# Kernel tuning notes

Measured on AMD Instinct MI355X. Metric: run time of the kernel, lower is better.

The kernel has to match this reference:

```python
import jax, jax.numpy as jnp
import numpy as np

THRESHOLD = 0.5
NEG_POS = 3
ALPHA = 1.0


def cxcy_to_xy(c):
    return jnp.concatenate([c[..., :2] - c[..., 2:] / 2, c[..., :2] + c[..., 2:] / 2], -1)


def xy_to_cxcy(b):
    return jnp.concatenate([(b[..., :2] + b[..., 2:]) / 2, b[..., 2:] - b[..., :2]], -1)


def compute_iou(a, b):
    # a: (M,4) xyxy, b: (D,4) xyxy -> (M,D)
    lt = jnp.maximum(a[:, None, :2], b[None, :, :2])
    rb = jnp.minimum(a[:, None, 2:], b[None, :, 2:])
    wh = jnp.clip(rb - lt, 0.0)
    inter = wh[..., 0] * wh[..., 1]
    area_a = (a[:, 2] - a[:, 0]) * (a[:, 3] - a[:, 1])
    area_b = (b[:, 2] - b[:, 0]) * (b[:, 3] - b[:, 1])
    return inter / (area_a[:, None] + area_b[None, :] - inter)


def encode_bboxes(g_cxcy, priors_cxcy):
    # standard SSD encoding with variances (0.1, 0.2)
    return jnp.concatenate([
        (g_cxcy[:, :2] - priors_cxcy[:, :2]) / (priors_cxcy[:, 2:] / 10.0),
        jnp.log(g_cxcy[:, 2:] / priors_cxcy[:, 2:]) * 5.0,
    ], -1)


def match_one(boxes, labels, priors_xy, priors_cxcy):
    # boxes: (M,4) xyxy, labels: (M,)
    M = boxes.shape[0]
    overlaps = compute_iou(boxes, priors_xy)                 # (M, D)
    overlaps_per_default = overlaps.max(axis=0)              # (D,)
    objects_per_default = overlaps.argmax(axis=0)            # (D,)
    defaults_per_gt = overlaps.argmax(axis=1)                # (M,)
    # force-match each gt to its best prior
    objects_per_default = objects_per_default.at[defaults_per_gt].set(jnp.arange(M))
    overlaps_per_default = overlaps_per_default.at[defaults_per_gt].set(1.0)
    lab = labels[objects_per_default]                        # (D,)
    lab = jnp.where(overlaps_per_default < THRESHOLD, 0, lab)
    matched = boxes[objects_per_default]                     # (D,4)
    loc_t = encode_bboxes(xy_to_cxcy(matched), priors_cxcy)  # (D,4)
    return loc_t, lab


def setup_inputs() -> dict:
    key = jax.random.key(0)
    ks = jax.random.split(key, 7)
    B, D, M, C = 128, 8732, 32, 21
    p_c = jax.random.uniform(ks[0], (D, 2), minval=0.05, maxval=0.95)
    p_wh = jax.random.uniform(ks[1], (D, 2), minval=0.02, maxval=0.4)
    default_boxes = jnp.concatenate([p_c, p_wh], -1)         # cxcy priors
    g_c = jax.random.uniform(ks[2], (B, M, 2), minval=0.2, maxval=0.8)
    g_wh = jax.random.uniform(ks[3], (B, M, 2), minval=0.05, maxval=0.3)
    gt_boxes = jnp.clip(jnp.concatenate([g_c - g_wh / 2, g_c + g_wh / 2], -1), 0.0, 1.0)
    gt_labels = jax.random.randint(ks[4], (B, M), 1, C)
    loc_pred = jax.random.normal(ks[5], (B, D, 4), dtype=jnp.float32)
    cls_pred = jax.random.normal(ks[6], (B, D, C), dtype=jnp.float32)
    return {"loc_pred": loc_pred, "cls_pred": cls_pred, "gt_boxes": gt_boxes,
            "gt_labels": gt_labels, "default_boxes": default_boxes}


def reference(loc_pred, cls_pred, gt_boxes, gt_labels, default_boxes):
    priors_xy = cxcy_to_xy(default_boxes)
    loc_t, conf_t = jax.vmap(match_one, in_axes=(0, 0, None, None))(
        gt_boxes, gt_labels, priors_xy, default_boxes)      # (B,D,4), (B,D)
    pos = conf_t > 0                                         # (B,D)
    n_pos = pos.sum(axis=1)                                  # (B,)
    n_total = jnp.maximum(n_pos.sum(), 1).astype(loc_pred.dtype)

    # localization: smooth-L1 summed over positives
    d = loc_pred - loc_t
    ad = jnp.abs(d)
    sl1 = jnp.where(ad < 1.0, 0.5 * d * d, ad - 0.5).sum(-1)  # (B,D)
    loc_loss = jnp.where(pos, sl1, 0.0).sum()

    # confidence: CE with hard negative mining (neg:pos = 3)
    logp = jax.nn.log_softmax(cls_pred, axis=-1)
    ce = -jnp.take_along_axis(logp, conf_t[..., None], axis=-1)[..., 0]  # (B,D)
    ce_neg = jnp.where(pos, 0.0, ce)
    order = jnp.argsort(-ce_neg, axis=1)
    rank = jnp.argsort(order, axis=1)                        # hardness rank per row
    n_neg = NEG_POS * n_pos                                  # (B,)
    neg_mask = (rank < n_neg[:, None]) & (~pos)
    conf_loss = jnp.where(pos | neg_mask, ce, 0.0).sum()

    return (conf_loss + ALPHA * loc_loss) / n_total
```

## Files before the change

### kernel.cpp

```cpp
#include <hip/hip_runtime.h>

#define BB 128
#define DD 8732
#define MM 32
#define CC 21

constexpr int K1_PR  = 4;
constexpr int K1_CH  = 256 * K1_PR;
constexpr int K1_NCH = (DD + K1_CH - 1) / K1_CH;
constexpr int K2_CELLS = 256;
constexpr int K2_NBLK  = (DD + K2_CELLS - 1) / K2_CELLS;
constexpr int K2B_T    = 1024;
constexpr int K2B_PER  = (DD + K2B_T - 1) / K2B_T;
constexpr int K2B_W    = K2B_T / 64;

constexpr size_t WS_DPG    = 0;
constexpr size_t WS_ROW    = 32768;
constexpr int    ROW_STRIDE = 16;
constexpr size_t WS_GSUM   = 40960;
constexpr size_t WS_GNPOS  = 41088;
constexpr size_t WS_DONE   = 41216;
constexpr size_t WS_ZERO_BYTES = 41344;
constexpr size_t WS_PACKED = 41472;
constexpr size_t WS_CENEG  = WS_PACKED + (size_t)BB * DD * 4;

__device__ __forceinline__ float wave_sum_f(float v) {
#pragma unroll
  for (int o = 32; o > 0; o >>= 1) v += __shfl_xor(v, o, 64);
  return v;
}
__device__ __forceinline__ int wave_sum_i(int v) {
#pragma unroll
  for (int o = 32; o > 0; o >>= 1) v += __shfl_xor(v, o, 64);
  return v;
}

__global__ __launch_bounds__(256) void k1_match(
    const float* __restrict__ gt_boxes, const int* __restrict__ gt_labels,
    const float* __restrict__ dboxes,
    unsigned int* __restrict__ packed, unsigned long long* __restrict__ dpg) {
  __shared__ float s_gx1[MM], s_gy1[MM], s_gx2[MM], s_gy2[MM], s_ga[MM];
  __shared__ int s_gl[MM];
  __shared__ unsigned long long s_pm[MM * 4];

  const int b = blockIdx.y;
  const int tid = threadIdx.x;
  if (tid < MM) {
    const float* g = gt_boxes + ((size_t)b * MM + tid) * 4;
    const float x1 = g[0], y1 = g[1], x2 = g[2], y2 = g[3];
    s_gx1[tid] = x1; s_gy1[tid] = y1; s_gx2[tid] = x2; s_gy2[tid] = y2;
    s_ga[tid] = __fmul_rn(__fsub_rn(x2, x1), __fsub_rn(y2, y1));
    s_gl[tid] = gt_labels[b * MM + tid];
  }
  __syncthreads();

  float px1[K1_PR], py1[K1_PR], px2[K1_PR], py2[K1_PR], pa[K1_PR];
  int dd[K1_PR];
  const int dbase = blockIdx.x * K1_CH + tid;
#pragma unroll
  for (int i = 0; i < K1_PR; ++i) {
    const int d = dbase + i * 256;
    if (d < DD) {
      const float4 p = *(const float4*)(dboxes + (size_t)d * 4);
      const float hw = __fmul_rn(p.z, 0.5f), hh = __fmul_rn(p.w, 0.5f);
      px1[i] = __fsub_rn(p.x, hw); py1[i] = __fsub_rn(p.y, hh);
      px2[i] = __fadd_rn(p.x, hw); py2[i] = __fadd_rn(p.y, hh);
      pa[i] = __fmul_rn(__fsub_rn(px2[i], px1[i]), __fsub_rn(py2[i], py1[i]));
      dd[i] = d;
    } else {
      px1[i] = 3e9f; py1[i] = 3e9f; px2[i] = 3e9f; py2[i] = 3e9f; pa[i] = 1.0f;
      dd[i] = 0x7FFFFFFF;
    }
  }

  float vb[K1_PR]; int mb[K1_PR];
#pragma unroll
  for (int i = 0; i < K1_PR; ++i) { vb[i] = -1.0f; mb[i] = 0; }

  const int lane = tid & 63, wid = tid >> 6;
  for (int m = 0; m < MM; ++m) {
    const float gx1 = s_gx1[m], gy1 = s_gy1[m], gx2 = s_gx2[m], gy2 = s_gy2[m];
    const float ga = s_ga[m];
    float mv = -1.0f; int md = 0x7FFFFFFF;
#pragma unroll
    for (int i = 0; i < K1_PR; ++i) {
      const float w = fmaxf(0.0f, __fsub_rn(fminf(gx2, px2[i]), fmaxf(gx1, px1[i])));
      const float h = fmaxf(0.0f, __fsub_rn(fminf(gy2, py2[i]), fmaxf(gy1, py1[i])));
      const float inter = __fmul_rn(w, h);
      const float den = __fsub_rn(__fadd_rn(ga, pa[i]), inter);
      const float val = __fdiv_rn(inter, den);
      if (val > vb[i]) { vb[i] = val; mb[i] = m; }
      if (val > mv) { mv = val; md = dd[i]; }
    }
    unsigned long long key =
        (((unsigned long long)__float_as_uint(mv)) << 32) |
        (unsigned long long)(0xFFFFFFFFu - (unsigned)md);
#pragma unroll
    for (int o = 32; o > 0; o >>= 1) {
      const unsigned long long other = __shfl_xor(key, o, 64);
      if (other > key) key = other;
    }
    if (lane == 0) s_pm[m * 4 + wid] = key;
  }
  __syncthreads();
  if (tid < MM) {
    unsigned long long k0 = s_pm[tid * 4 + 0];
    if (s_pm[tid * 4 + 1] > k0) k0 = s_pm[tid * 4 + 1];
    if (s_pm[tid * 4 + 2] > k0) k0 = s_pm[tid * 4 + 2];
    if (s_pm[tid * 4 + 3] > k0) k0 = s_pm[tid * 4 + 3];
    atomicMax(&dpg[b * MM + tid], k0);
  }
#pragma unroll
  for (int i = 0; i < K1_PR; ++i) {
    if (dd[i] < DD) {
      const int lab = (vb[i] < 0.5f) ? 0 : s_gl[mb[i]];
      packed[(size_t)b * DD + dd[i]] = ((unsigned)lab << 8) | (unsigned)mb[i];
    }
  }
}

__global__ __launch_bounds__(256) void k2a_ce(
    const float* __restrict__ loc_pred, const float* __restrict__ cls_pred,
    const float* __restrict__ gt_boxes, const int* __restrict__ gt_labels,
    const float* __restrict__ dboxes, const unsigned int* __restrict__ packed,
    const unsigned long long* __restrict__ dpg, float* __restrict__ ce_neg,
    float* __restrict__ rowacc) {
  __shared__ float s_cls[K2_CELLS * CC];
  __shared__ int s_dstar[MM], s_lab[MM];
  __shared__ float s_gt[MM][4];
  __shared__ float s_rf[4], s_rl[4];
  __shared__ int s_ri[4];

  const int b = blockIdx.y;
  const int d0 = blockIdx.x * K2_CELLS;
  const int tid = threadIdx.x;
  const int ncell = min(K2_CELLS, DD - d0);
  const int nflt = ncell * CC;
  const float* srcf = cls_pred + ((size_t)b * DD + d0) * CC;
  const int nv4 = nflt >> 2;
  for (int i = tid; i < nv4; i += 256)
    ((float4*)s_cls)[i] = ((const float4*)srcf)[i];
  for (int i = (nv4 << 2) + tid; i < nflt; i += 256) s_cls[i] = srcf[i];

  if (tid < MM) {
    s_dstar[tid] = (int)(0xFFFFFFFFu - (unsigned)(dpg[b * MM + tid] & 0xFFFFFFFFull));
    s_lab[tid] = gt_labels[b * MM + tid];
    const float4 g = *(const float4*)(gt_boxes + ((size_t)b * MM + tid) * 4);
    s_gt[tid][0] = g.x; s_gt[tid][1] = g.y; s_gt[tid][2] = g.z; s_gt[tid][3] = g.w;
  }
  __syncthreads();

  float ce_pos = 0.0f, sl1 = 0.0f; int posc = 0;
  if (tid < ncell) {
    const int d = d0 + tid;
    const unsigned p = packed[(size_t)b * DD + d];
    int bm = (int)(p & 255u), lab = (int)(p >> 8);
#pragma unroll
    for (int m = 0; m < MM; ++m)
      if (s_dstar[m] == d) { bm = m; lab = s_lab[m]; }
    const float* x = &s_cls[tid * CC];
    float mx = x[0];
#pragma unroll
    for (int c = 1; c < CC; ++c) mx = fmaxf(mx, x[c]);
    float se = 0.0f;
#pragma unroll
    for (int c = 0; c < CC; ++c) se = __fadd_rn(se, __expf(__fsub_rn(x[c], mx)));
    const float ce = __fsub_rn(__fadd_rn(mx, __logf(se)), x[lab]);
    const bool pos = lab > 0;
    ce_neg[(size_t)b * DD + d] = pos ? -1.0f : ce;
    if (pos) {
      posc = 1; ce_pos = ce;
      const float4 lp = *(const float4*)(loc_pred + ((size_t)b * DD + d) * 4);
      const float4 pr = *(const float4*)(dboxes + (size_t)d * 4);
      const float gx1 = s_gt[bm][0], gy1 = s_gt[bm][1];
      const float gx2 = s_gt[bm][2], gy2 = s_gt[bm][3];
      const float gcx = __fmul_rn(__fadd_rn(gx1, gx2), 0.5f);
      const float gcy = __fmul_rn(__fadd_rn(gy1, gy2), 0.5f);
      const float gw = __fsub_rn(gx2, gx1), gh = __fsub_rn(gy2, gy1);
      const float t0 = __fdiv_rn(__fsub_rn(gcx, pr.x), __fdiv_rn(pr.z, 10.0f));
      const float t1 = __fdiv_rn(__fsub_rn(gcy, pr.y), __fdiv_rn(pr.w, 10.0f));
      const float t2 = __fmul_rn(__logf(__fdiv_rn(gw, pr.z)), 5.0f);
      const float t3 = __fmul_rn(__logf(__fdiv_rn(gh, pr.w)), 5.0f);
      float dv, ad;
      dv = __fsub_rn(lp.x, t0); ad = fabsf(dv);
      sl1 += (ad < 1.0f) ? __fmul_rn(0.5f, __fmul_rn(dv, dv)) : __fsub_rn(ad, 0.5f);
      dv = __fsub_rn(lp.y, t1); ad = fabsf(dv);
      sl1 += (ad < 1.0f) ? __fmul_rn(0.5f, __fmul_rn(dv, dv)) : __fsub_rn(ad, 0.5f);
      dv = __fsub_rn(lp.z, t2); ad = fabsf(dv);
      sl1 += (ad < 1.0f) ? __fmul_rn(0.5f, __fmul_rn(dv, dv)) : __fsub_rn(ad, 0.5f);
      dv = __fsub_rn(lp.w, t3); ad = fabsf(dv);
      sl1 += (ad < 1.0f) ? __fmul_rn(0.5f, __fmul_rn(dv, dv)) : __fsub_rn(ad, 0.5f);
    }
  }
  const float cs = wave_sum_f(ce_pos);
  const float ls = wave_sum_f(sl1);
  const int ps = wave_sum_i(posc);
  const int lane = tid & 63, wid = tid >> 6;
  if (lane == 0) { s_rf[wid] = cs; s_rl[wid] = ls; s_ri[wid] = ps; }
  __syncthreads();
  if (tid == 0) {
    const float c = s_rf[0] + s_rf[1] + s_rf[2] + s_rf[3];
    const float l = s_rl[0] + s_rl[1] + s_rl[2] + s_rl[3];
    const int p = s_ri[0] + s_ri[1] + s_ri[2] + s_ri[3];
    float* row = rowacc + b * ROW_STRIDE;
    atomicAdd(&row[0], c);
    atomicAdd(&row[1], l);
    if (p) atomicAdd((int*)&row[2], p);
  }
}

__global__ __launch_bounds__(K2B_T) void k2b_topk(
    const float* __restrict__ ce_neg, const float* __restrict__ rowacc,
    float* __restrict__ gsum, int* __restrict__ gnpos,
    unsigned int* __restrict__ done, float* __restrict__ out) {
  __shared__ int s_ri[K2B_W];
  __shared__ float s_rf[K2B_W];
  const int b = blockIdx.x;
  const int tid = threadIdx.x;
  const int lane = tid & 63, wid = tid >> 6;
  const float* row = rowacc + b * ROW_STRIDE;
  const int np = ((const int*)row)[2];
  const int k = min(3 * np, DD - np);

  unsigned key[K2B_PER];
#pragma unroll
  for (int i = 0; i < K2B_PER; ++i) {
    const int d = tid + i * K2B_T;
    if (d < DD) {
      const unsigned u = __float_as_uint(ce_neg[(size_t)b * DD + d]);
      key[i] = (u & 0x80000000u) ? ~u : (u | 0x80000000u);
    } else key[i] = 0u;
  }

  float topk_sum = 0.0f;
  if (k > 0) {
    unsigned T = 0u;
    for (int bit = 31; bit >= 0; --bit) {
      const unsigned cand = T | (1u << bit);
      int c = 0;
#pragma unroll
      for (int i = 0; i < K2B_PER; ++i) c += (key[i] >= cand) ? 1 : 0;
      c = wave_sum_i(c);
      if (lane == 0) s_ri[wid] = c;
      __syncthreads();
      int total = 0;
#pragma unroll
      for (int w = 0; w < K2B_W; ++w) total += s_ri[w];
      __syncthreads();
      if (total >= k) T = cand;
    }
    int c = 0; float s = 0.0f;
#pragma unroll
    for (int i = 0; i < K2B_PER; ++i) {
      if (key[i] > T) { c += 1; s += __uint_as_float(key[i] ^ 0x80000000u); }
    }
    c = wave_sum_i(c); s = wave_sum_f(s);
    if (lane == 0) { s_ri[wid] = c; s_rf[wid] = s; }
    __syncthreads();
    if (tid == 0) {
      int cg = 0; float sg = 0.0f;
#pragma unroll
      for (int w = 0; w < K2B_W; ++w) { cg += s_ri[w]; sg += s_rf[w]; }
      const float vT = __uint_as_float(T ^ 0x80000000u);
      topk_sum = sg + (float)(k - cg) * vT;
    }
  }
  if (tid == 0) {
    atomicAdd(gsum, row[0] + row[1] + topk_sum);
    atomicAdd(gnpos, np);
    __threadfence();
    const unsigned old = atomicAdd(done, 1u);
    if (old == BB - 1) {
      const float total = atomicAdd(gsum, 0.0f);
      const int npt = atomicAdd(gnpos, 0);
      const float nt = (float)((npt > 0) ? npt : 1);
      out[0] = __fdiv_rn(total, nt);
    }
  }
}

extern "C" void kernel_launch(void* const* d_in, const int* in_sizes, int n_in,
                              void* d_out, int out_size, void* d_ws, size_t ws_size,
                              hipStream_t stream) {
  const float* loc_pred = (const float*)d_in[0];
  const float* cls_pred = (const float*)d_in[1];
  const float* gt_boxes = (const float*)d_in[2];
  const int* gt_labels = (const int*)d_in[3];
  const float* dboxes = (const float*)d_in[4];

  char* ws = (char*)d_ws;
  unsigned long long* dpg = (unsigned long long*)(ws + WS_DPG);
  float* rowacc = (float*)(ws + WS_ROW);
  float* gsum = (float*)(ws + WS_GSUM);
  int* gnpos = (int*)(ws + WS_GNPOS);
  unsigned int* done = (unsigned int*)(ws + WS_DONE);
  unsigned int* packed = (unsigned int*)(ws + WS_PACKED);
  float* ce_neg = (float*)(ws + WS_CENEG);

  hipMemsetAsync(ws, 0, WS_ZERO_BYTES, stream);

  k1_match<<<dim3(K1_NCH, BB), 256, 0, stream>>>(gt_boxes, gt_labels, dboxes,
                                                 packed, dpg);
  k2a_ce<<<dim3(K2_NBLK, BB), 256, 0, stream>>>(loc_pred, cls_pred, gt_boxes,
                                                gt_labels, dboxes, packed, dpg,
                                                ce_neg, rowacc);
  k2b_topk<<<BB, K2B_T, 0, stream>>>(ce_neg, rowacc, gsum, gnpos, done,
                                     (float*)d_out);
}
```

Baseline: 234.9 us.

## Fuse CE and top-k kernels with last-block radix select per row

Merges the CE/loc kernel and the top-k kernel into one launch: the last block to finish each row (tracked by a per-row atomic counter) performs the hard-negative selection. Selection switches from a 32-pass bitwise threshold search to a 4-pass 8-bit radix histogram select in shared memory, reusing the cls staging buffer through a union. It also replaces the per-cell 32-way forced-match scan with a shared override table, and splits the 64-bit shuffle argmax in the match kernel into float-max and index-min shuffles. This removes one kernel launch and many block-wide barriers. The cost is that the serial tail of each row runs in a single 256-thread block, and it adds extra fences and atomics.

```diff
diff --git a/kernel.cpp b/kernel.cpp
--- a/kernel.cpp
+++ b/kernel.cpp
@@ -10,9 +10,7 @@
 constexpr int K1_NCH = (DD + K1_CH - 1) / K1_CH;
 constexpr int K2_CELLS = 256;
 constexpr int K2_NBLK  = (DD + K2_CELLS - 1) / K2_CELLS;
-constexpr int K2B_T    = 1024;
-constexpr int K2B_PER  = (DD + K2B_T - 1) / K2B_T;
-constexpr int K2B_W    = K2B_T / 64;
+constexpr int K2T_PER  = (DD + K2_CELLS - 1) / K2_CELLS;
 
 constexpr size_t WS_DPG    = 0;
 constexpr size_t WS_ROW    = 32768;
@@ -20,8 +18,9 @@
 constexpr size_t WS_GSUM   = 40960;
 constexpr size_t WS_GNPOS  = 41088;
 constexpr size_t WS_DONE   = 41216;
-constexpr size_t WS_ZERO_BYTES = 41344;
-constexpr size_t WS_PACKED = 41472;
+constexpr size_t WS_RDONE  = 41344;
+constexpr size_t WS_ZERO_BYTES = 41856;
+constexpr size_t WS_PACKED = 41984;
 constexpr size_t WS_CENEG  = WS_PACKED + (size_t)BB * DD * 4;
 
 __device__ __forceinline__ float wave_sum_f(float v) {
@@ -92,15 +91,16 @@
       if (val > vb[i]) { vb[i] = val; mb[i] = m; }
       if (val > mv) { mv = val; md = dd[i]; }
     }
-    unsigned long long key =
-        (((unsigned long long)__float_as_uint(mv)) << 32) |
-        (unsigned long long)(0xFFFFFFFFu - (unsigned)md);
-#pragma unroll
-    for (int o = 32; o > 0; o >>= 1) {
-      const unsigned long long other = __shfl_xor(key, o, 64);
-      if (other > key) key = other;
-    }
-    if (lane == 0) s_pm[m * 4 + wid] = key;
+    float mva = mv;
+#pragma unroll
+    for (int o = 32; o > 0; o >>= 1) mva = fmaxf(mva, __shfl_xor(mva, o, 64));
+    int mdm = (mv == mva) ? md : 0x7FFFFFFF;
+#pragma unroll
+    for (int o = 32; o > 0; o >>= 1) mdm = min(mdm, __shfl_xor(mdm, o, 64));
+    if (lane == 0)
+      s_pm[m * 4 + wid] =
+          (((unsigned long long)__float_as_uint(mva)) << 32) |
+          (unsigned long long)(0xFFFFFFFFu - (unsigned)mdm);
   }
   __syncthreads();
   if (tid < MM) {
@@ -119,34 +119,51 @@
   }
 }
 
-__global__ __launch_bounds__(256) void k2a_ce(
+union K2Shared {
+  float cls[K2_CELLS * CC];
+  float4 cls4[(K2_CELLS * CC) / 4];
+  struct { int hist[16 * 256]; int bin[256]; int sel[2]; } r;
+};
+
+__global__ __launch_bounds__(256) void k2_fused(
     const float* __restrict__ loc_pred, const float* __restrict__ cls_pred,
     const float* __restrict__ gt_boxes, const int* __restrict__ gt_labels,
     const float* __restrict__ dboxes, const unsigned int* __restrict__ packed,
     const unsigned long long* __restrict__ dpg, float* __restrict__ ce_neg,
-    float* __restrict__ rowacc) {
-  __shared__ float s_cls[K2_CELLS * CC];
-  __shared__ int s_dstar[MM], s_lab[MM];
+    float* __restrict__ rowacc, unsigned int* __restrict__ rowdone,
+    float* __restrict__ gsum, int* __restrict__ gnpos,
+    unsigned int* __restrict__ done, float* __restrict__ out) {
+  __shared__ K2Shared u;
+  __shared__ int s_lab[MM];
   __shared__ float s_gt[MM][4];
+  __shared__ int s_ov[K2_CELLS];
   __shared__ float s_rf[4], s_rl[4];
   __shared__ int s_ri[4];
+  __shared__ int s_lastf, s_np;
 
   const int b = blockIdx.y;
   const int d0 = blockIdx.x * K2_CELLS;
   const int tid = threadIdx.x;
+  const int lane = tid & 63, wid = tid >> 6;
   const int ncell = min(K2_CELLS, DD - d0);
   const int nflt = ncell * CC;
   const float* srcf = cls_pred + ((size_t)b * DD + d0) * CC;
   const int nv4 = nflt >> 2;
-  for (int i = tid; i < nv4; i += 256)
-    ((float4*)s_cls)[i] = ((const float4*)srcf)[i];
-  for (int i = (nv4 << 2) + tid; i < nflt; i += 256) s_cls[i] = srcf[i];
-
+  for (int i = tid; i < nv4; i += 256) u.cls4[i] = ((const float4*)srcf)[i];
+  for (int i = (nv4 << 2) + tid; i < nflt; i += 256) u.cls[i] = srcf[i];
+  s_ov[tid] = 0;
+
+  int dstar = -1;
   if (tid < MM) {
-    s_dstar[tid] = (int)(0xFFFFFFFFu - (unsigned)(dpg[b * MM + tid] & 0xFFFFFFFFull));
+    dstar = (int)(0xFFFFFFFFu - (unsigned)(dpg[(size_t)b * MM + tid] & 0xFFFFFFFFull));
     s_lab[tid] = gt_labels[b * MM + tid];
     const float4 g = *(const float4*)(gt_boxes + ((size_t)b * MM + tid) * 4);
     s_gt[tid][0] = g.x; s_gt[tid][1] = g.y; s_gt[tid][2] = g.z; s_gt[tid][3] = g.w;
+  }
+  __syncthreads();
+  if (tid < MM) {
+    const int ds = dstar - d0;
+    if (ds >= 0 && ds < K2_CELLS) atomicMax(&s_ov[ds], tid + 1);
   }
   __syncthreads();
 
@@ -155,10 +172,9 @@
     const int d = d0 + tid;
     const unsigned p = packed[(size_t)b * DD + d];
     int bm = (int)(p & 255u), lab = (int)(p >> 8);
-#pragma unroll
-    for (int m = 0; m < MM; ++m)
-      if (s_dstar[m] == d) { bm = m; lab = s_lab[m]; }
-    const float* x = &s_cls[tid * CC];
+    const int ov = s_ov[tid];
+    if (ov) { bm = ov - 1; lab = s_lab[bm]; }
+    const float* x = &u.cls[tid * CC];
     float mx = x[0];
 #pragma unroll
     for (int c = 1; c < CC; ++c) mx = fmaxf(mx, x[c]);
@@ -195,86 +211,105 @@
   const float cs = wave_sum_f(ce_pos);
   const float ls = wave_sum_f(sl1);
   const int ps = wave_sum_i(posc);
-  const int lane = tid & 63, wid = tid >> 6;
   if (lane == 0) { s_rf[wid] = cs; s_rl[wid] = ls; s_ri[wid] = ps; }
   __syncthreads();
+  float* row = rowacc + b * ROW_STRIDE;
   if (tid == 0) {
     const float c = s_rf[0] + s_rf[1] + s_rf[2] + s_rf[3];
     const float l = s_rl[0] + s_rl[1] + s_rl[2] + s_rl[3];
-    const int p = s_ri[0] + s_ri[1] + s_ri[2] + s_ri[3];
-    float* row = rowacc + b * ROW_STRIDE;
+    const int p2 = s_ri[0] + s_ri[1] + s_ri[2] + s_ri[3];
     atomicAdd(&row[0], c);
     atomicAdd(&row[1], l);
-    if (p) atomicAdd((int*)&row[2], p);
-  }
-}
-
-__global__ __launch_bounds__(K2B_T) void k2b_topk(
-    const float* __restrict__ ce_neg, const float* __restrict__ rowacc,
-    float* __restrict__ gsum, int* __restrict__ gnpos,
-    unsigned int* __restrict__ done, float* __restrict__ out) {
-  __shared__ int s_ri[K2B_W];
-  __shared__ float s_rf[K2B_W];
-  const int b = blockIdx.x;
-  const int tid = threadIdx.x;
-  const int lane = tid & 63, wid = tid >> 6;
-  const float* row = rowacc + b * ROW_STRIDE;
-  const int np = ((const int*)row)[2];
+    if (p2) atomicAdd((int*)&row[2], p2);
+    int lastf = 0;
+    __threadfence();
+    if (atomicAdd(&rowdone[b], 1u) == K2_NBLK - 1) {
+      __threadfence();
+      lastf = 1;
+      s_np = ((const int*)row)[2];
+    }
+    s_lastf = lastf;
+  }
+  __syncthreads();
+  if (!s_lastf) return;
+
+  const int np = s_np;
   const int k = min(3 * np, DD - np);
-
-  unsigned key[K2B_PER];
-#pragma unroll
-  for (int i = 0; i < K2B_PER; ++i) {
-    const int d = tid + i * K2B_T;
-    if (d < DD) {
-      const unsigned u = __float_as_uint(ce_neg[(size_t)b * DD + d]);
-      key[i] = (u & 0x80000000u) ? ~u : (u | 0x80000000u);
-    } else key[i] = 0u;
-  }
-
-  float topk_sum = 0.0f;
+  const float* cerow = ce_neg + (size_t)b * DD;
+  unsigned key[K2T_PER];
+#pragma unroll
+  for (int i = 0; i < K2T_PER; ++i) {
+    const int d = tid + i * K2_CELLS;
+    unsigned uu = 0xFF800000u;
+    if (d < DD) uu = __float_as_uint(cerow[d]);
+    key[i] = (uu & 0x80000000u) ? ~uu : (uu | 0x80000000u);
+  }
+
+  unsigned T = 0u; int kk = k; float topk = 0.0f;
   if (k > 0) {
-    unsigned T = 0u;
-    for (int bit = 31; bit >= 0; --bit) {
-      const unsigned cand = T | (1u << bit);
-      int c = 0;
-#pragma unroll
-      for (int i = 0; i < K2B_PER; ++i) c += (key[i] >= cand) ? 1 : 0;
-      c = wave_sum_i(c);
-      if (lane == 0) s_ri[wid] = c;
+    for (int r = 0; r < 4; ++r) {
+      const int shift = 24 - 8 * r;
+      const unsigned pmask = (r == 0) ? 0u : (0xFFFFFFFFu << (32 - 8 * r));
+      for (int i = tid; i < 16 * 256; i += 256) u.r.hist[i] = 0;
       __syncthreads();
-      int total = 0;
-#pragma unroll
-      for (int w = 0; w < K2B_W; ++w) total += s_ri[w];
+      int* h = u.r.hist + ((tid & 15) << 8);
+      const unsigned want = T & pmask;
+#pragma unroll
+      for (int i = 0; i < K2T_PER; ++i)
+        if ((key[i] & pmask) == want) atomicAdd(&h[(key[i] >> shift) & 255], 1);
       __syncthreads();
-      if (total >= k) T = cand;
-    }
-    int c = 0; float s = 0.0f;
-#pragma unroll
-    for (int i = 0; i < K2B_PER; ++i) {
-      if (key[i] > T) { c += 1; s += __uint_as_float(key[i] ^ 0x80000000u); }
-    }
-    c = wave_sum_i(c); s = wave_sum_f(s);
-    if (lane == 0) { s_ri[wid] = c; s_rf[wid] = s; }
+      int bt = 0;
+#pragma unroll
+      for (int s2 = 0; s2 < 16; ++s2) bt += u.r.hist[(s2 << 8) + tid];
+      u.r.bin[tid] = bt;
+      __syncthreads();
+      if (tid < 64) {
+        const int h0 = u.r.bin[4 * tid], h1 = u.r.bin[4 * tid + 1];
+        const int h2 = u.r.bin[4 * tid + 2], h3 = u.r.bin[4 * tid + 3];
+        const int gsv = h0 + h1 + h2 + h3;
+        int sfx = gsv;
+#pragma unroll
+        for (int o = 1; o < 64; o <<= 1) {
+          const int x = __shfl_down(sfx, o, 64);
+          if (tid + o < 64) sfx += x;
+        }
+        const int above = sfx - gsv;
+        if (sfx >= kk && above < kk) {
+          const int c3 = above + h3, c2 = c3 + h2, c1 = c2 + h1;
+          int v, cgt;
+          if (c3 >= kk)      { v = 3; cgt = above; }
+          else if (c2 >= kk) { v = 2; cgt = c3; }
+          else if (c1 >= kk) { v = 1; cgt = c2; }
+          else               { v = 0; cgt = c1; }
+          u.r.sel[0] = (tid << 2) + v;
+          u.r.sel[1] = kk - cgt;
+        }
+      }
+      __syncthreads();
+      T |= ((unsigned)u.r.sel[0]) << shift;
+      kk = u.r.sel[1];
+    }
+    float sv = 0.0f;
+#pragma unroll
+    for (int i = 0; i < K2T_PER; ++i)
+      if (key[i] > T) sv += __uint_as_float(key[i] ^ 0x80000000u);
+    sv = wave_sum_f(sv);
+    if (lane == 0) s_rf[wid] = sv;
     __syncthreads();
     if (tid == 0) {
-      int cg = 0; float sg = 0.0f;
-#pragma unroll
-      for (int w = 0; w < K2B_W; ++w) { cg += s_ri[w]; sg += s_rf[w]; }
-      const float vT = __uint_as_float(T ^ 0x80000000u);
-      topk_sum = sg + (float)(k - cg) * vT;
+      const float vT = (T & 0x80000000u) ? __uint_as_float(T ^ 0x80000000u)
+                                         : __uint_as_float(~T);
+      topk = (s_rf[0] + s_rf[1] + s_rf[2] + s_rf[3]) + (float)kk * vT;
     }
   }
   if (tid == 0) {
-    atomicAdd(gsum, row[0] + row[1] + topk_sum);
+    atomicAdd(gsum, row[0] + row[1] + topk);
     atomicAdd(gnpos, np);
     __threadfence();
-    const unsigned old = atomicAdd(done, 1u);
-    if (old == BB - 1) {
+    if (atomicAdd(done, 1u) == BB - 1) {
       const float total = atomicAdd(gsum, 0.0f);
       const int npt = atomicAdd(gnpos, 0);
-      const float nt = (float)((npt > 0) ? npt : 1);
-      out[0] = __fdiv_rn(total, nt);
+      out[0] = __fdiv_rn(total, (float)((npt > 0) ? npt : 1));
     }
   }
 }
@@ -294,6 +329,7 @@
   float* gsum = (float*)(ws + WS_GSUM);
   int* gnpos = (int*)(ws + WS_GNPOS);
   unsigned int* done = (unsigned int*)(ws + WS_DONE);
+  unsigned int* rowdone = (unsigned int*)(ws + WS_RDONE);
   unsigned int* packed = (unsigned int*)(ws + WS_PACKED);
   float* ce_neg = (float*)(ws + WS_CENEG);
 
@@ -301,9 +337,9 @@
 
   k1_match<<<dim3(K1_NCH, BB), 256, 0, stream>>>(gt_boxes, gt_labels, dboxes,
                                                  packed, dpg);
-  k2a_ce<<<dim3(K2_NBLK, BB), 256, 0, stream>>>(loc_pred, cls_pred, gt_boxes,
-                                                gt_labels, dboxes, packed, dpg,
-                                                ce_neg, rowacc);
-  k2b_topk<<<BB, K2B_T, 0, stream>>>(ce_neg, rowacc, gsum, gnpos, done,
-                                     (float*)d_out);
-}
+  k2_fused<<<dim3(K2_NBLK, BB), 256, 0, stream>>>(loc_pred, cls_pred, gt_boxes,
+                                                  gt_labels, dboxes, packed, dpg,
+                                                  ce_neg, rowacc, rowdone,
+                                                  gsum, gnpos, done,
+                                                  (float*)d_out);
+}
```

After: 442.9 us. +88.5%, slower.
